# Optimization experiments

Measured on AMD Instinct MI355X. Metric: run time of the kernel, lower is better.

The kernel has to match this reference:

```python
import math
import jax, jax.numpy as jnp
import numpy as np

B, S, HID, H, NREL = 4, 512, 1024, 16, 64
D = HID // H  # per-head size = 64, must equal relation embedding dim


def setup_inputs() -> dict:
    key = jax.random.key(0)
    ks = jax.random.split(key, 12)
    w = lambda k, shape: jax.random.normal(k, shape, jnp.float32) * 0.02
    return {
        "q_in": jax.random.normal(ks[0], (B, S, HID), jnp.float32),
        "k_in": jax.random.normal(ks[1], (B, S, HID), jnp.float32),
        "v_in": jax.random.normal(ks[2], (B, S, HID), jnp.float32),
        "mask": jax.random.randint(ks[3], (B, 1, S, S), 0, NREL),
        "Wq": w(ks[4], (HID, HID)), "bq": jnp.zeros((HID,), jnp.float32),
        "Wk": w(ks[5], (HID, HID)), "bk": jnp.zeros((HID,), jnp.float32),
        "Wv": w(ks[6], (HID, HID)), "bv": jnp.zeros((HID,), jnp.float32),
        "Wo": w(ks[7], (HID, HID)), "bo": jnp.zeros((HID,), jnp.float32),
        "rel_k_table": w(ks[8], (NREL, D)),
        "rel_v_table": w(ks[9], (NREL, D)),
    }


def reference(q_in, k_in, v_in, mask, Wq, bq, Wk, bk, Wv, bv, Wo, bo,
              rel_k_table, rel_v_table):
    def proj(x, W, b):  # [B,S,HID] -> [B,H,S,D]
        return (x @ W.T + b).reshape(B, S, H, D).transpose(0, 2, 1, 3)

    q = proj(q_in, Wq, bq)
    k = proj(k_in, Wk, bk)
    v = proj(v_in, Wv, bv)

    ids = mask[:, 0]                      # [B,S,S] relation ids
    rel_k = rel_k_table[ids]              # [B,S,S,D]
    rel_v = rel_v_table[ids]              # [B,S,S,D]

    scores = jnp.einsum('bhqd,bhkd->bhqk', q, k)
    scores = scores + jnp.einsum('bhqd,bqkd->bhqk', q, rel_k) / 4.0
    scores = scores / math.sqrt(float(D))

    bias = (1.0 - (mask > 0).astype(scores.dtype)) * -10000.0  # [B,1,S,S]
    probs = jax.nn.softmax(scores + bias, axis=-1)             # [B,H,S,S]

    out = jnp.einsum('bhqk,bhkd->bhqd', probs, v)
    out = out + 0.25 * jnp.einsum('bhqk,bqkd->bhqd', probs, rel_v)
    out = out.transpose(0, 2, 1, 3).reshape(B, S, HID)
    return out @ Wo.T + bo
```

## Files before the change

### kernel.cpp

```cpp
#include <hip/hip_runtime.h>


typedef __attribute__((ext_vector_type(8))) short bf16x8 __attribute__((may_alias));
typedef __attribute__((ext_vector_type(4))) float f32x4;

__device__ __forceinline__ short f2bf(float x) {
    unsigned u = __float_as_uint(x);
    u += 0x7fff + ((u >> 16) & 1);
    return (short)(u >> 16);
}

__device__ __forceinline__ void async16(void* lds, const void* g) {
    __builtin_amdgcn_global_load_lds(
        (const __attribute__((address_space(1))) void*)g,
        (__attribute__((address_space(3))) void*)lds, 16, 0, 0);
}

__global__ __launch_bounds__(256)
void cast_all(const float* __restrict__ x0, const float* __restrict__ x1, const float* __restrict__ x2,
              const float* __restrict__ w0, const float* __restrict__ w1,
              const float* __restrict__ w2, const float* __restrict__ w3,
              short* __restrict__ y0, short* __restrict__ y1, short* __restrict__ y2,
              short* __restrict__ u0, short* __restrict__ u1,
              short* __restrict__ u2, short* __restrict__ u3)
{
    size_t i = (size_t)blockIdx.x * 256 + threadIdx.x;
    const float* src; short* dst; size_t off;
    if (i < 3u*524288u) {
        int s = (int)(i / 524288u); off = i % 524288u;
        src = s == 0 ? x0 : (s == 1 ? x1 : x2);
        dst = s == 0 ? y0 : (s == 1 ? y1 : y2);
    } else {
        size_t j = i - 3u*524288u;
        int s = (int)(j / 262144u); off = j % 262144u;
        src = s == 0 ? w0 : (s == 1 ? w1 : (s == 2 ? w2 : w3));
        dst = s == 0 ? u0 : (s == 1 ? u1 : (s == 2 ? u2 : u3));
    }
    float4 f = ((const float4*)src)[off];
    short4 o; o.x = f2bf(f.x); o.y = f2bf(f.y); o.z = f2bf(f.z); o.w = f2bf(f.w);
    ((short4*)dst)[off] = o;
}

__global__ __launch_bounds__(256)
void gemm128(const short* __restrict__ A0, const short* __restrict__ A1, const short* __restrict__ A2,
             const short* __restrict__ B0, const short* __restrict__ B1, const short* __restrict__ B2,
             const float* __restrict__ c0, const float* __restrict__ c1, const float* __restrict__ c2,
             void* __restrict__ O0, void* __restrict__ O1, void* __restrict__ O2,
             int mode)
{
    __shared__ short ldsw[4 * 8192];

    const int z = blockIdx.z;
    const short* A    = z == 0 ? A0 : (z == 1 ? A1 : A2);
    const short* Bm   = z == 0 ? B0 : (z == 1 ? B1 : B2);
    const float* bias = z == 0 ? c0 : (z == 1 ? c1 : c2);
    void*        O    = z == 0 ? O0 : (z == 1 ? O1 : O2);

    const int t = threadIdx.x;
    const int lane = t & 63, w = t >> 6;
    const int wr = w >> 1, wc = w & 1;
    const int quad = lane >> 4, cl = lane & 15;
    const int rowBase = blockIdx.y * 128;
    const int colBase = blockIdx.x * 128;
    const int gl = ((lane & 7) - (lane >> 3)) & 7;

    f32x4 acc[4][4];
#pragma unroll
    for (int i = 0; i < 4; ++i)
#pragma unroll
        for (int j = 0; j < 4; ++j) acc[i][j] = (f32x4){0.f, 0.f, 0.f, 0.f};

    const int rstage = w * 8 + (lane >> 3);
    const short* Ag = A  + (size_t)(rowBase + rstage) * 1024 + gl * 8;
    const short* Bg = Bm + (size_t)(colBase + rstage) * 1024 + gl * 8;

    {
        short* Als = ldsw;
        short* Bls = ldsw + 8192;
#pragma unroll
        for (int i = 0; i < 4; ++i)
            async16(&Als[(i * 32 + w * 8) * 64], Ag + (size_t)i * 32 * 1024);
#pragma unroll
        for (int i = 0; i < 4; ++i)
            async16(&Bls[(i * 32 + w * 8) * 64], Bg + (size_t)i * 32 * 1024);
    }

    for (int it = 0; it < 16; ++it) {
        const int cur = it & 1;
        __syncthreads();
        if (it < 15) {
            short* Als = ldsw + (cur ^ 1) * 16384;
            short* Bls = Als + 8192;
            const int k0 = (it + 1) * 64;
#pragma unroll
            for (int i = 0; i < 4; ++i)
                async16(&Als[(i * 32 + w * 8) * 64], Ag + (size_t)i * 32 * 1024 + k0);
#pragma unroll
            for (int i = 0; i < 4; ++i)
                async16(&Bls[(i * 32 + w * 8) * 64], Bg + (size_t)i * 32 * 1024 + k0);
        }
        const short* Als = ldsw + cur * 16384;
        const short* Bls = Als + 8192;
#pragma unroll
        for (int kk = 0; kk < 2; ++kk) {
            bf16x8 a[4], b[4];
#pragma unroll
            for (int mi = 0; mi < 4; ++mi) {
                int r = wr * 64 + mi * 16 + cl;
                int s = (kk * 4 + quad + r) & 7;
                a[mi] = *(const bf16x8*)&Als[r * 64 + s * 8];
            }
#pragma unroll
            for (int ni = 0; ni < 4; ++ni) {
                int r = wc * 64 + ni * 16 + cl;
                int s = (kk * 4 + quad + r) & 7;
                b[ni] = *(const bf16x8*)&Bls[r * 64 + s * 8];
            }
#pragma unroll
            for (int mi = 0; mi < 4; ++mi)
#pragma unroll
                for (int ni = 0; ni < 4; ++ni)
                    acc[mi][ni] = __builtin_amdgcn_mfma_f32_16x16x32_bf16(
                        a[mi], b[ni], acc[mi][ni], 0, 0, 0);
        }
    }

    if (mode == 0) {
#pragma unroll
        for (int mi = 0; mi < 4; ++mi)
#pragma unroll
            for (int ni = 0; ni < 4; ++ni) {
                int col = colBase + wc * 64 + ni * 16 + cl;
                float bv = bias[col];
#pragma unroll
                for (int reg = 0; reg < 4; ++reg) {
                    int row = rowBase + wr * 64 + mi * 16 + quad * 4 + reg;
                    ((float*)O)[(size_t)row * 1024 + col] = acc[mi][ni][reg] + bv;
                }
            }
        return;
    }

    __syncthreads();
    short* Tls = ldsw;
    if (z == 2) {
#pragma unroll
        for (int mi = 0; mi < 4; ++mi)
#pragma unroll
            for (int ni = 0; ni < 4; ++ni) {
                int d = wc * 64 + ni * 16 + cl;
                float bv = bias[colBase + d];
                short4 pk;
                pk.x = f2bf(acc[mi][ni][0] + bv);
                pk.y = f2bf(acc[mi][ni][1] + bv);
                pk.z = f2bf(acc[mi][ni][2] + bv);
                pk.w = f2bf(acc[mi][ni][3] + bv);
                int sl = wr * 64 + mi * 16 + quad * 4;
                *(short4*)&Tls[d * 136 + sl] = pk;
            }
        __syncthreads();
        int dl = t >> 4, sl8 = (t & 15) * 8;
        int bb = rowBase >> 9, sBase = rowBase & 511, hh0 = colBase >> 6;
#pragma unroll
        for (int dd = 0; dd < 8; ++dd) {
            int d_local = dd * 16 + dl;
            int hh = hh0 + (d_local >> 6), d = d_local & 63;
            short* dst = (short*)O + (((size_t)(bb * 16 + hh) * 64 + d) << 9) + sBase + sl8;
            *(bf16x8*)dst = *(const bf16x8*)&Tls[d_local * 136 + sl8];
        }
    } else {
#pragma unroll
        for (int mi = 0; mi < 4; ++mi)
#pragma unroll
            for (int ni = 0; ni < 4; ++ni) {
                int d = wc * 64 + ni * 16 + cl;
                float bv = bias[colBase + d];
#pragma unroll
                for (int reg = 0; reg < 4; ++reg) {
                    int sl = wr * 64 + mi * 16 + quad * 4 + reg;
                    Tls[sl * 136 + d] = f2bf(acc[mi][ni][reg] + bv);
                }
            }
        __syncthreads();
        int sl = t >> 1, half = t & 1;
        int bb = rowBase >> 9, sBase = rowBase & 511, hh = (colBase >> 6) + half;
        short* dst = (short*)O + (((size_t)(bb * 16 + hh) * 512 + sBase + sl) << 6);
#pragma unroll
        for (int j = 0; j < 8; ++j)
            *(bf16x8*)(dst + j * 8) = *(const bf16x8*)&Tls[sl * 136 + half * 64 + j * 8];
    }
}

#define A_OFF_BINS 4352
#define A_OFF_OACC 8704
#define A_OFF_LACC 13056
#define A_OFF_INVL 13120
#define A_OFF_PST  13184
#define A_LDS_TOT  22400

__global__ __launch_bounds__(256)
void attn_kernel(const short* __restrict__ qg, const short* __restrict__ kg,
                 const short* __restrict__ vtg, const int* __restrict__ mask,
                 const float* __restrict__ relk, const float* __restrict__ relv,
                 short* __restrict__ attn_b)
{
    __shared__ __align__(16) char pool[A_LDS_TOT];
    float* qwr    = (float*)pool;
    short* binsBf = (short*)pool;
    float* bins   = (float*)(pool + A_OFF_BINS);
    float* Oacc   = (float*)(pool + A_OFF_OACC);
    float* Lacc   = (float*)(pool + A_OFF_LACC);
    float* invl   = (float*)(pool + A_OFF_INVL);

    const int t = threadIdx.x, lane = t & 63, w = t >> 6;
    const int quad = lane >> 4, cl = lane & 15;
    const int bid = blockIdx.x, qbk = bid & 31, bh = bid >> 5;
    const int b = bh >> 4, h = bh & 15, q0 = qbk * 16;

    const short* qbase = qg  + ((size_t)bh * 512 + q0) * 64;
    const short* kbase = kg  + (size_t)bh * 512 * 64;
    const short* vbase = vtg + (size_t)bh * 64 * 512;
    const int*   mb    = mask + (size_t)b * 512 * 512 + (size_t)q0 * 512;

    short* Pst = (short*)(pool + A_OFF_PST + w * 2304);

    for (int i = t; i < (A_OFF_PST - A_OFF_BINS) / 4; i += 256)
        bins[i] = 0.f;

    bf16x8 rvb0, rvb1;
    {
        const float* rp = relv + (size_t)(quad * 8) * 64 + w * 16 + cl;
#pragma unroll
        for (int j = 0; j < 8; ++j) rvb0[j] = f2bf(rp[j * 64]);
#pragma unroll
        for (int j = 0; j < 8; ++j) rvb1[j] = f2bf(rp[2048 + j * 64]);
    }

    bf16x8 qa0 = *(const bf16x8*)(qbase + cl * 64 + quad * 8);
    bf16x8 qa1 = *(const bf16x8*)(qbase + cl * 64 + 32 + quad * 8);

    {
        const float* kp = relk + (size_t)(w * 16 + cl) * 64 + quad * 8;
        bf16x8 rb0, rb1;
#pragma unroll
        for (int j = 0; j < 8; ++j) rb0[j] = f2bf(kp[j]);
#pragma unroll
        for (int j = 0; j < 8; ++j) rb1[j] = f2bf(kp[32 + j]);
        f32x4 qr = (f32x4){0.f, 0.f, 0.f, 0.f};
        qr = __builtin_amdgcn_mfma_f32_16x16x32_bf16(qa0, rb0, qr, 0, 0, 0);
        qr = __builtin_amdgcn_mfma_f32_16x16x32_bf16(qa1, rb1, qr, 0, 0, 0);
#pragma unroll
        for (int reg = 0; reg < 4; ++reg)
            qwr[(quad * 4 + reg) * 68 + w * 16 + cl] = qr[reg];
    }
    __syncthreads();

    f32x4 oacc[4];
#pragma unroll
    for (int dt = 0; dt < 4; ++dt) oacc[dt] = (f32x4){0.f, 0.f, 0.f, 0.f};
    float lpart[4] = {0.f, 0.f, 0.f, 0.f};

#pragma unroll
    for (int c = 0; c < 2; ++c) {
        const int k0 = w * 128 + c * 64;
#pragma unroll
        for (int nt = 0; nt < 4; ++nt) {
            const int kidx = k0 + nt * 16 + cl;
            const short* kp = kbase + (size_t)kidx * 64 + quad * 8;
            bf16x8 kb0 = *(const bf16x8*)kp;
            bf16x8 kb1 = *(const bf16x8*)(kp + 32);
            f32x4 s = (f32x4){0.f, 0.f, 0.f, 0.f};
            s = __builtin_amdgcn_mfma_f32_16x16x32_bf16(qa0, kb0, s, 0, 0, 0);
            s = __builtin_amdgcn_mfma_f32_16x16x32_bf16(qa1, kb1, s, 0, 0, 0);
#pragma unroll
            for (int reg = 0; reg < 4; ++reg) {
                int q = quad * 4 + reg;
                int id = mb[q * 512 + kidx];
                float sc = (s[reg] + 0.25f * qwr[q * 68 + id]) * 0.125f;
                sc = (id == 0) ? sc - 10000.f : sc;
                float p = __expf(sc);
                lpart[reg] += p;
                atomicAdd(&bins[q * 68 + id], p);
                Pst[q * 72 + nt * 16 + cl] = f2bf(p);
            }
        }
        bf16x8 pa0 = *(const bf16x8*)&Pst[cl * 72 + quad * 8];
        bf16x8 pa1 = *(const bf16x8*)&Pst[cl * 72 + 32 + quad * 8];
#pragma unroll
        for (int dt = 0; dt < 4; ++dt) {
            const short* vp = vbase + (size_t)(dt * 16 + cl) * 512 + k0 + quad * 8;
            bf16x8 vb0 = *(const bf16x8*)vp;
            bf16x8 vb1 = *(const bf16x8*)(vp + 32);
            oacc[dt] = __builtin_amdgcn_mfma_f32_16x16x32_bf16(pa0, vb0, oacc[dt], 0, 0, 0);
            oacc[dt] = __builtin_amdgcn_mfma_f32_16x16x32_bf16(pa1, vb1, oacc[dt], 0, 0, 0);
        }
    }

#pragma unroll
    for (int reg = 0; reg < 4; ++reg) {
        int q = quad * 4 + reg;
#pragma unroll
        for (int dt = 0; dt < 4; ++dt)
            atomicAdd(&Oacc[q * 68 + dt * 16 + cl], oacc[dt][reg]);
        float lsum = lpart[reg];
#pragma unroll
        for (int m = 8; m >= 1; m >>= 1) lsum += __shfl_xor(lsum, m);
        if (cl == 0) atomicAdd(&Lacc[q], lsum);
    }
    __syncthreads();

    if (t < 16) invl[t] = 1.0f / Lacc[t];
    {
        int q = t >> 4, r0 = (t & 15) * 4;
        float4 f = *(const float4*)&bins[q * 68 + r0];
        short4 o;
        o.x = f2bf(f.x); o.y = f2bf(f.y); o.z = f2bf(f.z); o.w = f2bf(f.w);
        *(short4*)&binsBf[q * 72 + r0] = o;
    }
    __syncthreads();

    bf16x8 ba0 = *(const bf16x8*)&binsBf[cl * 72 + quad * 8];
    bf16x8 ba1 = *(const bf16x8*)&binsBf[cl * 72 + 32 + quad * 8];
    f32x4 racc = (f32x4){0.f, 0.f, 0.f, 0.f};
    racc = __builtin_amdgcn_mfma_f32_16x16x32_bf16(ba0, rvb0, racc, 0, 0, 0);
    racc = __builtin_amdgcn_mfma_f32_16x16x32_bf16(ba1, rvb1, racc, 0, 0, 0);

#pragma unroll
    for (int reg = 0; reg < 4; ++reg) {
        int q = quad * 4 + reg;
        int d = w * 16 + cl;
        float val = (Oacc[q * 68 + d] + 0.25f * racc[reg]) * invl[q];
        attn_b[(size_t)(b * 512 + q0 + q) * 1024 + h * 64 + d] = f2bf(val);
    }
}

extern "C" void kernel_launch(void* const* d_in, const int* in_sizes, int n_in,
                              void* d_out, int out_size, void* d_ws, size_t ws_size,
                              hipStream_t stream)
{
    const float* q_in = (const float*)d_in[0];
    const float* k_in = (const float*)d_in[1];
    const float* v_in = (const float*)d_in[2];
    const int*   mask = (const int*)d_in[3];
    const float* Wq   = (const float*)d_in[4];
    const float* bq   = (const float*)d_in[5];
    const float* Wk   = (const float*)d_in[6];
    const float* bk   = (const float*)d_in[7];
    const float* Wv   = (const float*)d_in[8];
    const float* bv   = (const float*)d_in[9];
    const float* Wo   = (const float*)d_in[10];
    const float* bo   = (const float*)d_in[11];
    const float* relk = (const float*)d_in[12];
    const float* relv = (const float*)d_in[13];

    char* ws = (char*)d_ws;
    short* qb     = (short*)(ws);
    short* kb     = (short*)(ws + (4u  << 20));
    short* vt     = (short*)(ws + (8u  << 20));
    short* attn_b = (short*)(ws + (12u << 20));
    short* Xq     = (short*)(ws + (16u << 20));
    short* Xk     = (short*)(ws + (20u << 20));
    short* Xv     = (short*)(ws + (24u << 20));
    short* Wqb    = (short*)(ws + (28u << 20));
    short* Wkb    = (short*)(ws + (30u << 20));
    short* Wvb    = (short*)(ws + (32u << 20));
    short* Wob    = (short*)(ws + (34u << 20));

    cast_all<<<10240, 256, 0, stream>>>(q_in, k_in, v_in, Wq, Wk, Wv, Wo,
                                        Xq, Xk, Xv, Wqb, Wkb, Wvb, Wob);

    gemm128<<<dim3(8, 16, 3), 256, 0, stream>>>(
        Xq, Xk, Xv, Wqb, Wkb, Wvb, bq, bk, bv, qb, kb, vt, 1);

    attn_kernel<<<dim3(2048), 256, 0, stream>>>(qb, kb, vt, mask, relk, relv, attn_b);

    gemm128<<<dim3(8, 16, 1), 256, 0, stream>>>(
        attn_b, attn_b, attn_b, Wob, Wob, Wob, bo, bo, bo,
        (void*)d_out, (void*)d_out, (void*)d_out, 0);
}
```

Baseline: 279.6 us.

## Shrink GEMM tiles to 128x64 and run attention with one wave per block

The projection and output GEMMs now use 128x64 tiles, which doubles the grid to fill more CUs and reduces LDS use per block. The attention kernel is restructured so a single 64-thread wave handles all 512 keys for a 16-query block. This removes the cross-wave LDS atomics, the Oacc/Lacc reductions and the block barriers, and it remaps block ids so heads are interleaved. In exchange each wave does 8 sequential chunks with less parallelism per block, and masked probabilities are now written as exact zero instead of exp(score-10000).

```diff
diff --git a/kernel.cpp b/kernel.cpp
--- a/kernel.cpp
+++ b/kernel.cpp
@@ -42,13 +42,13 @@
 }
 
 __global__ __launch_bounds__(256)
-void gemm128(const short* __restrict__ A0, const short* __restrict__ A1, const short* __restrict__ A2,
-             const short* __restrict__ B0, const short* __restrict__ B1, const short* __restrict__ B2,
-             const float* __restrict__ c0, const float* __restrict__ c1, const float* __restrict__ c2,
-             void* __restrict__ O0, void* __restrict__ O1, void* __restrict__ O2,
-             int mode)
+void gemm12864(const short* __restrict__ A0, const short* __restrict__ A1, const short* __restrict__ A2,
+               const short* __restrict__ B0, const short* __restrict__ B1, const short* __restrict__ B2,
+               const float* __restrict__ c0, const float* __restrict__ c1, const float* __restrict__ c2,
+               void* __restrict__ O0, void* __restrict__ O1, void* __restrict__ O2,
+               int mode)
 {
-    __shared__ short ldsw[4 * 8192];
+    __shared__ short ldsw[2 * 12288];
 
     const int z = blockIdx.z;
     const short* A    = z == 0 ? A0 : (z == 1 ? A1 : A2);
@@ -61,14 +61,14 @@
     const int wr = w >> 1, wc = w & 1;
     const int quad = lane >> 4, cl = lane & 15;
     const int rowBase = blockIdx.y * 128;
-    const int colBase = blockIdx.x * 128;
+    const int colBase = blockIdx.x * 64;
     const int gl = ((lane & 7) - (lane >> 3)) & 7;
 
-    f32x4 acc[4][4];
+    f32x4 acc[4][2];
 #pragma unroll
     for (int i = 0; i < 4; ++i)
 #pragma unroll
-        for (int j = 0; j < 4; ++j) acc[i][j] = (f32x4){0.f, 0.f, 0.f, 0.f};
+        for (int j = 0; j < 2; ++j) acc[i][j] = (f32x4){0.f, 0.f, 0.f, 0.f};
 
     const int rstage = w * 8 + (lane >> 3);
     const short* Ag = A  + (size_t)(rowBase + rstage) * 1024 + gl * 8;
@@ -81,7 +81,7 @@
         for (int i = 0; i < 4; ++i)
             async16(&Als[(i * 32 + w * 8) * 64], Ag + (size_t)i * 32 * 1024);
 #pragma unroll
-        for (int i = 0; i < 4; ++i)
+        for (int i = 0; i < 2; ++i)
             async16(&Bls[(i * 32 + w * 8) * 64], Bg + (size_t)i * 32 * 1024);
     }
 
@@ -89,21 +89,21 @@
         const int cur = it & 1;
         __syncthreads();
         if (it < 15) {
-            short* Als = ldsw + (cur ^ 1) * 16384;
+            short* Als = ldsw + (cur ^ 1) * 12288;
             short* Bls = Als + 8192;
             const int k0 = (it + 1) * 64;
 #pragma unroll
             for (int i = 0; i < 4; ++i)
                 async16(&Als[(i * 32 + w * 8) * 64], Ag + (size_t)i * 32 * 1024 + k0);
 #pragma unroll
-            for (int i = 0; i < 4; ++i)
+            for (int i = 0; i < 2; ++i)
                 async16(&Bls[(i * 32 + w * 8) * 64], Bg + (size_t)i * 32 * 1024 + k0);
         }
-        const short* Als = ldsw + cur * 16384;
+        const short* Als = ldsw + cur * 12288;
         const short* Bls = Als + 8192;
 #pragma unroll
         for (int kk = 0; kk < 2; ++kk) {
-            bf16x8 a[4], b[4];
+            bf16x8 a[4], b[2];
 #pragma unroll
             for (int mi = 0; mi < 4; ++mi) {
                 int r = wr * 64 + mi * 16 + cl;
@@ -111,15 +111,15 @@
                 a[mi] = *(const bf16x8*)&Als[r * 64 + s * 8];
             }
 #pragma unroll
-            for (int ni = 0; ni < 4; ++ni) {
-                int r = wc * 64 + ni * 16 + cl;
+            for (int ni = 0; ni < 2; ++ni) {
+                int r = wc * 32 + ni * 16 + cl;
                 int s = (kk * 4 + quad + r) & 7;
                 b[ni] = *(const bf16x8*)&Bls[r * 64 + s * 8];
             }
 #pragma unroll
             for (int mi = 0; mi < 4; ++mi)
 #pragma unroll
-                for (int ni = 0; ni < 4; ++ni)
+                for (int ni = 0; ni < 2; ++ni)
                     acc[mi][ni] = __builtin_amdgcn_mfma_f32_16x16x32_bf16(
                         a[mi], b[ni], acc[mi][ni], 0, 0, 0);
         }
@@ -129,8 +129,8 @@
 #pragma unroll
         for (int mi = 0; mi < 4; ++mi)
 #pragma unroll
-            for (int ni = 0; ni < 4; ++ni) {
-                int col = colBase + wc * 64 + ni * 16 + cl;
+            for (int ni = 0; ni < 2; ++ni) {
+                int col = colBase + wc * 32 + ni * 16 + cl;
                 float bv = bias[col];
 #pragma unroll
                 for (int reg = 0; reg < 4; ++reg) {
@@ -147,8 +147,8 @@
 #pragma unroll
         for (int mi = 0; mi < 4; ++mi)
 #pragma unroll
-            for (int ni = 0; ni < 4; ++ni) {
-                int d = wc * 64 + ni * 16 + cl;
+            for (int ni = 0; ni < 2; ++ni) {
+                int d = wc * 32 + ni * 16 + cl;
                 float bv = bias[colBase + d];
                 short4 pk;
                 pk.x = f2bf(acc[mi][ni][0] + bv);
@@ -159,62 +159,55 @@
                 *(short4*)&Tls[d * 136 + sl] = pk;
             }
         __syncthreads();
-        int dl = t >> 4, sl8 = (t & 15) * 8;
-        int bb = rowBase >> 9, sBase = rowBase & 511, hh0 = colBase >> 6;
-#pragma unroll
-        for (int dd = 0; dd < 8; ++dd) {
-            int d_local = dd * 16 + dl;
-            int hh = hh0 + (d_local >> 6), d = d_local & 63;
-            short* dst = (short*)O + (((size_t)(bb * 16 + hh) * 64 + d) << 9) + sBase + sl8;
-            *(bf16x8*)dst = *(const bf16x8*)&Tls[d_local * 136 + sl8];
-        }
+        int d = t >> 2, s0 = (t & 3) * 32;
+        int bb = rowBase >> 9, sBase = rowBase & 511, hh = colBase >> 6;
+        short* dst = (short*)O + (((size_t)(bb * 16 + hh) * 64 + d) << 9) + sBase + s0;
+#pragma unroll
+        for (int j = 0; j < 4; ++j)
+            *(bf16x8*)(dst + j * 8) = *(const bf16x8*)&Tls[d * 136 + s0 + j * 8];
     } else {
 #pragma unroll
         for (int mi = 0; mi < 4; ++mi)
 #pragma unroll
-            for (int ni = 0; ni < 4; ++ni) {
-                int d = wc * 64 + ni * 16 + cl;
+            for (int ni = 0; ni < 2; ++ni) {
+                int d = wc * 32 + ni * 16 + cl;
                 float bv = bias[colBase + d];
 #pragma unroll
                 for (int reg = 0; reg < 4; ++reg) {
                     int sl = wr * 64 + mi * 16 + quad * 4 + reg;
-                    Tls[sl * 136 + d] = f2bf(acc[mi][ni][reg] + bv);
+                    Tls[sl * 72 + d] = f2bf(acc[mi][ni][reg] + bv);
                 }
             }
         __syncthreads();
         int sl = t >> 1, half = t & 1;
-        int bb = rowBase >> 9, sBase = rowBase & 511, hh = (colBase >> 6) + half;
-        short* dst = (short*)O + (((size_t)(bb * 16 + hh) * 512 + sBase + sl) << 6);
-#pragma unroll
-        for (int j = 0; j < 8; ++j)
-            *(bf16x8*)(dst + j * 8) = *(const bf16x8*)&Tls[sl * 136 + half * 64 + j * 8];
-    }
-}
-
-#define A_OFF_BINS 4352
-#define A_OFF_OACC 8704
-#define A_OFF_LACC 13056
-#define A_OFF_INVL 13120
-#define A_OFF_PST  13184
-#define A_LDS_TOT  22400
-
-__global__ __launch_bounds__(256)
+        int bb = rowBase >> 9, sBase = rowBase & 511, hh = colBase >> 6;
+        short* dst = (short*)O + (((size_t)(bb * 16 + hh) * 512 + sBase + sl) << 6) + half * 32;
+#pragma unroll
+        for (int j = 0; j < 4; ++j)
+            *(bf16x8*)(dst + j * 8) = *(const bf16x8*)&Tls[sl * 72 + half * 32 + j * 8];
+    }
+}
+
+#define AT_BINS 4352
+#define AT_PST  8704
+#define AT_TOT  11264
+
+__global__ __launch_bounds__(64)
 void attn_kernel(const short* __restrict__ qg, const short* __restrict__ kg,
                  const short* __restrict__ vtg, const int* __restrict__ mask,
                  const float* __restrict__ relk, const float* __restrict__ relv,
                  short* __restrict__ attn_b)
 {
-    __shared__ __align__(16) char pool[A_LDS_TOT];
+    __shared__ __align__(16) char pool[AT_TOT];
     float* qwr    = (float*)pool;
-    short* binsBf = (short*)pool;
-    float* bins   = (float*)(pool + A_OFF_BINS);
-    float* Oacc   = (float*)(pool + A_OFF_OACC);
-    float* Lacc   = (float*)(pool + A_OFF_LACC);
-    float* invl   = (float*)(pool + A_OFF_INVL);
-
-    const int t = threadIdx.x, lane = t & 63, w = t >> 6;
+    float* bins   = (float*)(pool + AT_BINS);
+    short* Pst    = (short*)(pool + AT_PST);
+    short* binsBf = Pst;
+
+    const int lane = threadIdx.x;
     const int quad = lane >> 4, cl = lane & 15;
-    const int bid = blockIdx.x, qbk = bid & 31, bh = bid >> 5;
+    const int bid = blockIdx.x;
+    const int bh = bid & 63, qbk = bid >> 6;
     const int b = bh >> 4, h = bh & 15, q0 = qbk * 16;
 
     const short* qbase = qg  + ((size_t)bh * 512 + q0) * 64;
@@ -222,25 +215,14 @@
     const short* vbase = vtg + (size_t)bh * 64 * 512;
     const int*   mb    = mask + (size_t)b * 512 * 512 + (size_t)q0 * 512;
 
-    short* Pst = (short*)(pool + A_OFF_PST + w * 2304);
-
-    for (int i = t; i < (A_OFF_PST - A_OFF_BINS) / 4; i += 256)
-        bins[i] = 0.f;
-
-    bf16x8 rvb0, rvb1;
-    {
-        const float* rp = relv + (size_t)(quad * 8) * 64 + w * 16 + cl;
-#pragma unroll
-        for (int j = 0; j < 8; ++j) rvb0[j] = f2bf(rp[j * 64]);
-#pragma unroll
-        for (int j = 0; j < 8; ++j) rvb1[j] = f2bf(rp[2048 + j * 64]);
-    }
+    for (int i = lane; i < 16 * 68; i += 64) bins[i] = 0.f;
 
     bf16x8 qa0 = *(const bf16x8*)(qbase + cl * 64 + quad * 8);
     bf16x8 qa1 = *(const bf16x8*)(qbase + cl * 64 + 32 + quad * 8);
 
-    {
-        const float* kp = relk + (size_t)(w * 16 + cl) * 64 + quad * 8;
+#pragma unroll
+    for (int rt = 0; rt < 4; ++rt) {
+        const float* kp = relk + (size_t)(rt * 16 + cl) * 64 + quad * 8;
         bf16x8 rb0, rb1;
 #pragma unroll
         for (int j = 0; j < 8; ++j) rb0[j] = f2bf(kp[j]);
@@ -251,18 +233,16 @@
         qr = __builtin_amdgcn_mfma_f32_16x16x32_bf16(qa1, rb1, qr, 0, 0, 0);
 #pragma unroll
         for (int reg = 0; reg < 4; ++reg)
-            qwr[(quad * 4 + reg) * 68 + w * 16 + cl] = qr[reg];
-    }
-    __syncthreads();
+            qwr[(quad * 4 + reg) * 68 + rt * 16 + cl] = qr[reg];
+    }
 
     f32x4 oacc[4];
 #pragma unroll
     for (int dt = 0; dt < 4; ++dt) oacc[dt] = (f32x4){0.f, 0.f, 0.f, 0.f};
     float lpart[4] = {0.f, 0.f, 0.f, 0.f};
 
-#pragma unroll
-    for (int c = 0; c < 2; ++c) {
-        const int k0 = w * 128 + c * 64;
+    for (int c = 0; c < 8; ++c) {
+        const int k0 = c * 64;
 #pragma unroll
         for (int nt = 0; nt < 4; ++nt) {
             const int kidx = k0 + nt * 16 + cl;
@@ -277,8 +257,7 @@
                 int q = quad * 4 + reg;
                 int id = mb[q * 512 + kidx];
                 float sc = (s[reg] + 0.25f * qwr[q * 68 + id]) * 0.125f;
-                sc = (id == 0) ? sc - 10000.f : sc;
-                float p = __expf(sc);
+                float p = (id == 0) ? 0.f : __expf(sc);
                 lpart[reg] += p;
                 atomicAdd(&bins[q * 68 + id], p);
                 Pst[q * 72 + nt * 16 + cl] = f2bf(p);
@@ -296,41 +275,45 @@
         }
     }
 
+    float invq[4];
 #pragma unroll
     for (int reg = 0; reg < 4; ++reg) {
-        int q = quad * 4 + reg;
-#pragma unroll
-        for (int dt = 0; dt < 4; ++dt)
-            atomicAdd(&Oacc[q * 68 + dt * 16 + cl], oacc[dt][reg]);
-        float lsum = lpart[reg];
-#pragma unroll
-        for (int m = 8; m >= 1; m >>= 1) lsum += __shfl_xor(lsum, m);
-        if (cl == 0) atomicAdd(&Lacc[q], lsum);
-    }
-    __syncthreads();
-
-    if (t < 16) invl[t] = 1.0f / Lacc[t];
+        float l = lpart[reg];
+#pragma unroll
+        for (int m = 8; m >= 1; m >>= 1) l += __shfl_xor(l, m);
+        invq[reg] = 1.0f / l;
+    }
+
     {
-        int q = t >> 4, r0 = (t & 15) * 4;
-        float4 f = *(const float4*)&bins[q * 68 + r0];
-        short4 o;
-        o.x = f2bf(f.x); o.y = f2bf(f.y); o.z = f2bf(f.z); o.w = f2bf(f.w);
-        *(short4*)&binsBf[q * 72 + r0] = o;
-    }
-    __syncthreads();
+        int q = lane >> 2, r0 = (lane & 3) * 16;
+#pragma unroll
+        for (int j = 0; j < 4; ++j) {
+            float4 f = *(const float4*)&bins[q * 68 + r0 + j * 4];
+            short4 o;
+            o.x = f2bf(f.x); o.y = f2bf(f.y); o.z = f2bf(f.z); o.w = f2bf(f.w);
+            *(short4*)&binsBf[q * 72 + r0 + j * 4] = o;
+        }
+    }
 
     bf16x8 ba0 = *(const bf16x8*)&binsBf[cl * 72 + quad * 8];
     bf16x8 ba1 = *(const bf16x8*)&binsBf[cl * 72 + 32 + quad * 8];
-    f32x4 racc = (f32x4){0.f, 0.f, 0.f, 0.f};
-    racc = __builtin_amdgcn_mfma_f32_16x16x32_bf16(ba0, rvb0, racc, 0, 0, 0);
-    racc = __builtin_amdgcn_mfma_f32_16x16x32_bf16(ba1, rvb1, racc, 0, 0, 0);
-
-#pragma unroll
-    for (int reg = 0; reg < 4; ++reg) {
-        int q = quad * 4 + reg;
-        int d = w * 16 + cl;
-        float val = (Oacc[q * 68 + d] + 0.25f * racc[reg]) * invl[q];
-        attn_b[(size_t)(b * 512 + q0 + q) * 1024 + h * 64 + d] = f2bf(val);
+#pragma unroll
+    for (int dt = 0; dt < 4; ++dt) {
+        const float* rp = relv + (size_t)(quad * 8) * 64 + dt * 16 + cl;
+        bf16x8 rv0, rv1;
+#pragma unroll
+        for (int j = 0; j < 8; ++j) rv0[j] = f2bf(rp[j * 64]);
+#pragma unroll
+        for (int j = 0; j < 8; ++j) rv1[j] = f2bf(rp[2048 + j * 64]);
+        f32x4 racc = (f32x4){0.f, 0.f, 0.f, 0.f};
+        racc = __builtin_amdgcn_mfma_f32_16x16x32_bf16(ba0, rv0, racc, 0, 0, 0);
+        racc = __builtin_amdgcn_mfma_f32_16x16x32_bf16(ba1, rv1, racc, 0, 0, 0);
+#pragma unroll
+        for (int reg = 0; reg < 4; ++reg) {
+            int q = quad * 4 + reg;
+            float val = (oacc[dt][reg] + 0.25f * racc[reg]) * invq[reg];
+            attn_b[(size_t)(b * 512 + q0 + q) * 1024 + h * 64 + dt * 16 + cl] = f2bf(val);
+        }
     }
 }
 
@@ -369,12 +352,12 @@
     cast_all<<<10240, 256, 0, stream>>>(q_in, k_in, v_in, Wq, Wk, Wv, Wo,
                                         Xq, Xk, Xv, Wqb, Wkb, Wvb, Wob);
 
-    gemm128<<<dim3(8, 16, 3), 256, 0, stream>>>(
+    gemm12864<<<dim3(16, 16, 3), 256, 0, stream>>>(
         Xq, Xk, Xv, Wqb, Wkb, Wvb, bq, bk, bv, qb, kb, vt, 1);
 
-    attn_kernel<<<dim3(2048), 256, 0, stream>>>(qb, kb, vt, mask, relk, relv, attn_b);
-
-    gemm128<<<dim3(8, 16, 1), 256, 0, stream>>>(
+    attn_kernel<<<dim3(2048), 64, 0, stream>>>(qb, kb, vt, mask, relk, relv, attn_b);
+
+    gemm12864<<<dim3(16, 16, 1), 256, 0, stream>>>(
         attn_b, attn_b, attn_b, Wob, Wob, Wob, bo, bo, bo,
         (void*)d_out, (void*)d_out, (void*)d_out, 0);
 }
```

Result: faster. 239.0 us (-14.5%).
